# Optimization experiments

Measured on AMD Instinct MI355X. Metric: run time of the kernel, lower is better.

The kernel has to match this reference:

```python
import jax, jax.numpy as jnp
import numpy as np

N, E, D, H = 50000, 400000, 128, 256


def setup_inputs() -> dict:
    key = jax.random.key(0)
    ks = jax.random.split(key, 16)
    s = 0.02
    inp = {
        "x": jax.random.normal(ks[0], (N, D), dtype=jnp.float32),
        "edge_index": jax.random.randint(ks[1], (2, E), 0, N, dtype=jnp.int64),
        "steps": 1,
        # encoder MLP: Linear(D->H), Linear(H->H), relu after each
        "enc_w1": jax.random.normal(ks[2], (H, D), dtype=jnp.float32) * s,
        "enc_b1": jnp.zeros((H,), dtype=jnp.float32),
        "enc_w2": jax.random.normal(ks[3], (H, H), dtype=jnp.float32) * s,
        "enc_b2": jnp.zeros((H,), dtype=jnp.float32),
        # GeneralConv lin_msg (root_weight=False, bias=True)
        "msg_w": jax.random.normal(ks[4], (H, H), dtype=jnp.float32) * s,
        "msg_b": jnp.zeros((H,), dtype=jnp.float32),
        # decoder MLP: Linear(2H->H) relu, Linear(H->D) tanh
        "dec_w1": jax.random.normal(ks[5], (H, 2 * H), dtype=jnp.float32) * s,
        "dec_b1": jnp.zeros((H,), dtype=jnp.float32),
        "dec_w2": jax.random.normal(ks[6], (D, H), dtype=jnp.float32) * s,
        "dec_b2": jnp.zeros((D,), dtype=jnp.float32),
    }
    return inp


def reference(x, edge_index, steps, enc_w1, enc_b1, enc_w2, enc_b2,
              msg_w, msg_b, dec_w1, dec_b1, dec_w2, dec_b2):
    src = edge_index[0]
    dst = edge_index[1]
    n = x.shape[0]
    for _ in range(steps):  # steps is a small static python int
        # encoder MLP (batch_norm=False, dropout=0, relu + relu)
        h = jax.nn.relu(x @ enc_w1.T + enc_b1)
        h = jax.nn.relu(h @ enc_w2.T + enc_b2)
        # GeneralConv: message = lin_msg(x_j); aggr='add'; no root weight
        # lin_msg is edge-independent -> transform on nodes, then gather/scatter
        m = h @ msg_w.T + msg_b                      # [N, H]
        out = jax.ops.segment_sum(m[src], dst, num_segments=n)  # [N, H]
        # decoder on cat(out, h): relu then tanh
        d = jax.nn.relu(jnp.concatenate([out, h], axis=-1) @ dec_w1.T + dec_b1)
        x = jnp.tanh(d @ dec_w2.T + dec_b2)
    return x
```

## Files before the change

### kernel.cpp

```cpp
#include <hip/hip_runtime.h>
#include <cmath>


typedef __attribute__((ext_vector_type(8))) short  short8;
typedef __attribute__((ext_vector_type(4))) float  f32x4;
typedef __attribute__((ext_vector_type(4))) unsigned short us4;

typedef unsigned short u16;
typedef unsigned int   u32;

static __device__ __forceinline__ u16 f2bf(float f) {
    u32 u = __float_as_uint(f);
    u = (u + 0x7FFFu + ((u >> 16) & 1u)) >> 16;
    return (u16)u;
}
static __device__ __forceinline__ float bf2f(u16 h) {
    return __uint_as_float(((u32)h) << 16);
}

static __device__ __forceinline__ void g2l16(const void* g, void* l) {
    __builtin_amdgcn_global_load_lds(
        (const __attribute__((address_space(1))) u32*)g,
        (__attribute__((address_space(3))) u32*)l, 16, 0, 0);
}

__global__ __launch_bounds__(256, 2) void enc_fused(
    const u16* __restrict__ xb, const u16* __restrict__ w1,
    const float* __restrict__ b1, const u16* __restrict__ w2,
    const float* __restrict__ b2, const u16* __restrict__ wm,
    const float* __restrict__ bm, u16* __restrict__ hout,
    u16* __restrict__ mout, const int N)
{
    __shared__ u16 As[64 * 32];
    __shared__ u16 Ws[256 * 32];
    __shared__ u16 hL[8][64 * 32];

    const int t    = threadIdx.x;
    const int r0   = blockIdx.x * 64;
    const int wave = t >> 6;
    const int lane = t & 63;
    const int n    = lane & 15;
    const int q    = lane >> 4;
    const int wc   = wave * 64;
    const int lrow = lane >> 2;
    const int qofs = (lane & 3) * 8;

    const int arow = min(r0 + wave * 16 + lrow, N - 1);
    const u16* aptr = xb + (size_t)arow * 128 + qofs;

    int wrow[4];
#pragma unroll
    for (int k2 = 0; k2 < 4; k2++) wrow[k2] = (wave + 4 * k2) * 16 + lrow;

    f32x4 acc[4][4];
#pragma unroll
    for (int i = 0; i < 4; i++)
#pragma unroll
        for (int j = 0; j < 4; j++) acc[i][j] = (f32x4)0.0f;

    for (int kc = 0; kc < 128; kc += 32) {
        __syncthreads();
        g2l16(aptr + kc, &As[wave * 512]);
#pragma unroll
        for (int k2 = 0; k2 < 4; k2++)
            g2l16(w1 + (size_t)wrow[k2] * 128 + kc + qofs,
                  &Ws[(wave + 4 * k2) * 512]);
        __syncthreads();
        short8 af[4], bf[4];
#pragma unroll
        for (int i = 0; i < 4; i++)
            af[i] = *reinterpret_cast<const short8*>(&As[(i * 16 + n) * 32 + q * 8]);
#pragma unroll
        for (int j = 0; j < 4; j++)
            bf[j] = *reinterpret_cast<const short8*>(&Ws[(wc + j * 16 + n) * 32 + q * 8]);
#pragma unroll
        for (int i = 0; i < 4; i++)
#pragma unroll
            for (int j = 0; j < 4; j++)
                acc[i][j] = __builtin_amdgcn_mfma_f32_16x16x32_bf16(
                    af[i], bf[j], acc[i][j], 0, 0, 0);
    }
    {
        float bv[4];
#pragma unroll
        for (int j = 0; j < 4; j++) bv[j] = b1[wc + j * 16 + n];
#pragma unroll
        for (int i = 0; i < 4; i++)
#pragma unroll
            for (int reg = 0; reg < 4; reg++) {
                const int row = i * 16 + q * 4 + reg;
#pragma unroll
                for (int j = 0; j < 4; j++) {
                    const int col = wc + j * 16 + n;
                    const float v = fmaxf(acc[i][j][reg] + bv[j], 0.0f);
                    hL[col >> 5][row * 32 + (col & 31)] = f2bf(v);
                }
            }
    }

#pragma unroll
    for (int i = 0; i < 4; i++)
#pragma unroll
        for (int j = 0; j < 4; j++) acc[i][j] = (f32x4)0.0f;
    for (int c = 0; c < 8; c++) {
        __syncthreads();
#pragma unroll
        for (int k2 = 0; k2 < 4; k2++)
            g2l16(w2 + (size_t)wrow[k2] * 256 + c * 32 + qofs,
                  &Ws[(wave + 4 * k2) * 512]);
        __syncthreads();
        short8 af[4], bf[4];
#pragma unroll
        for (int i = 0; i < 4; i++)
            af[i] = *reinterpret_cast<const short8*>(&hL[c][(i * 16 + n) * 32 + q * 8]);
#pragma unroll
        for (int j = 0; j < 4; j++)
            bf[j] = *reinterpret_cast<const short8*>(&Ws[(wc + j * 16 + n) * 32 + q * 8]);
#pragma unroll
        for (int i = 0; i < 4; i++)
#pragma unroll
            for (int j = 0; j < 4; j++)
                acc[i][j] = __builtin_amdgcn_mfma_f32_16x16x32_bf16(
                    af[i], bf[j], acc[i][j], 0, 0, 0);
    }
    {
        float bv[4];
#pragma unroll
        for (int j = 0; j < 4; j++) bv[j] = b2[wc + j * 16 + n];
#pragma unroll
        for (int i = 0; i < 4; i++)
#pragma unroll
            for (int reg = 0; reg < 4; reg++) {
                const int row = r0 + i * 16 + q * 4 + reg;
                if (row < N) {
#pragma unroll
                    for (int j = 0; j < 4; j++) {
                        const float v = fmaxf(acc[i][j][reg] + bv[j], 0.0f);
                        hout[(size_t)row * 256 + wc + j * 16 + n] = f2bf(v);
                    }
                }
            }
        __syncthreads();
#pragma unroll
        for (int i = 0; i < 4; i++)
#pragma unroll
            for (int reg = 0; reg < 4; reg++) {
                const int row = i * 16 + q * 4 + reg;
#pragma unroll
                for (int j = 0; j < 4; j++) {
                    const int col = wc + j * 16 + n;
                    const float v = fmaxf(acc[i][j][reg] + bv[j], 0.0f);
                    hL[col >> 5][row * 32 + (col & 31)] = f2bf(v);
                }
            }
    }

#pragma unroll
    for (int i = 0; i < 4; i++)
#pragma unroll
        for (int j = 0; j < 4; j++) acc[i][j] = (f32x4)0.0f;
    for (int c = 0; c < 8; c++) {
        __syncthreads();
#pragma unroll
        for (int k2 = 0; k2 < 4; k2++)
            g2l16(wm + (size_t)wrow[k2] * 256 + c * 32 + qofs,
                  &Ws[(wave + 4 * k2) * 512]);
        __syncthreads();
        short8 af[4], bf[4];
#pragma unroll
        for (int i = 0; i < 4; i++)
            af[i] = *reinterpret_cast<const short8*>(&hL[c][(i * 16 + n) * 32 + q * 8]);
#pragma unroll
        for (int j = 0; j < 4; j++)
            bf[j] = *reinterpret_cast<const short8*>(&Ws[(wc + j * 16 + n) * 32 + q * 8]);
#pragma unroll
        for (int i = 0; i < 4; i++)
#pragma unroll
            for (int j = 0; j < 4; j++)
                acc[i][j] = __builtin_amdgcn_mfma_f32_16x16x32_bf16(
                    af[i], bf[j], acc[i][j], 0, 0, 0);
    }
    {
        float bv[4];
#pragma unroll
        for (int j = 0; j < 4; j++) bv[j] = bm[wc + j * 16 + n];
#pragma unroll
        for (int i = 0; i < 4; i++)
#pragma unroll
            for (int reg = 0; reg < 4; reg++) {
                const int row = r0 + i * 16 + q * 4 + reg;
                if (row < N) {
#pragma unroll
                    for (int j = 0; j < 4; j++)
                        mout[(size_t)row * 256 + wc + j * 16 + n] =
                            f2bf(acc[i][j][reg] + bv[j]);
                }
            }
    }
}

__global__ __launch_bounds__(256, 2) void dec_fused(
    const u16* __restrict__ aggr, const u16* __restrict__ h,
    const u16* __restrict__ wd1, const float* __restrict__ bd1,
    const u16* __restrict__ wd2, const float* __restrict__ bd2,
    float* __restrict__ out, const int N)
{
    __shared__ u16 As[64 * 32];
    __shared__ u16 Ws[256 * 32];
    __shared__ u16 dL[8][64 * 32];

    const int t    = threadIdx.x;
    const int r0   = blockIdx.x * 64;
    const int wave = t >> 6;
    const int lane = t & 63;
    const int n    = lane & 15;
    const int q    = lane >> 4;
    const int wc   = wave * 64;
    const int lrow = lane >> 2;
    const int qofs = (lane & 3) * 8;

    const int arow = min(r0 + wave * 16 + lrow, N - 1);
    const u16* ap0 = aggr + (size_t)arow * 256 + qofs;
    const u16* ap1 = h    + (size_t)arow * 256 + qofs;

    int wrow[4];
#pragma unroll
    for (int k2 = 0; k2 < 4; k2++) wrow[k2] = (wave + 4 * k2) * 16 + lrow;

    f32x4 acc[4][4];
#pragma unroll
    for (int i = 0; i < 4; i++)
#pragma unroll
        for (int j = 0; j < 4; j++) acc[i][j] = (f32x4)0.0f;

    for (int kc = 0; kc < 512; kc += 32) {
        __syncthreads();
        if (kc < 256) g2l16(ap0 + kc, &As[wave * 512]);
        else          g2l16(ap1 + (kc - 256), &As[wave * 512]);
#pragma unroll
        for (int k2 = 0; k2 < 4; k2++)
            g2l16(wd1 + (size_t)wrow[k2] * 512 + kc + qofs,
                  &Ws[(wave + 4 * k2) * 512]);
        __syncthreads();
        short8 af[4], bf[4];
#pragma unroll
        for (int i = 0; i < 4; i++)
            af[i] = *reinterpret_cast<const short8*>(&As[(i * 16 + n) * 32 + q * 8]);
#pragma unroll
        for (int j = 0; j < 4; j++)
            bf[j] = *reinterpret_cast<const short8*>(&Ws[(wc + j * 16 + n) * 32 + q * 8]);
#pragma unroll
        for (int i = 0; i < 4; i++)
#pragma unroll
            for (int j = 0; j < 4; j++)
                acc[i][j] = __builtin_amdgcn_mfma_f32_16x16x32_bf16(
                    af[i], bf[j], acc[i][j], 0, 0, 0);
    }
    {
        float bv[4];
#pragma unroll
        for (int j = 0; j < 4; j++) bv[j] = bd1[wc + j * 16 + n];
#pragma unroll
        for (int i = 0; i < 4; i++)
#pragma unroll
            for (int reg = 0; reg < 4; reg++) {
                const int row = i * 16 + q * 4 + reg;
#pragma unroll
                for (int j = 0; j < 4; j++) {
                    const int col = wc + j * 16 + n;
                    const float v = fmaxf(acc[i][j][reg] + bv[j], 0.0f);
                    dL[col >> 5][row * 32 + (col & 31)] = f2bf(v);
                }
            }
    }

    f32x4 acc2[4][2];
#pragma unroll
    for (int i = 0; i < 4; i++)
#pragma unroll
        for (int j = 0; j < 2; j++) acc2[i][j] = (f32x4)0.0f;
    const int wc2 = wave * 32;
    for (int c = 0; c < 8; c++) {
        __syncthreads();
        g2l16(wd2 + (size_t)(wave * 16 + lrow) * 256 + c * 32 + qofs,
              &Ws[wave * 512]);
        g2l16(wd2 + (size_t)((wave + 4) * 16 + lrow) * 256 + c * 32 + qofs,
              &Ws[(wave + 4) * 512]);
        __syncthreads();
        short8 af[4], bf[2];
#pragma unroll
        for (int i = 0; i < 4; i++)
            af[i] = *reinterpret_cast<const short8*>(&dL[c][(i * 16 + n) * 32 + q * 8]);
#pragma unroll
        for (int j = 0; j < 2; j++)
            bf[j] = *reinterpret_cast<const short8*>(&Ws[(wc2 + j * 16 + n) * 32 + q * 8]);
#pragma unroll
        for (int i = 0; i < 4; i++)
#pragma unroll
            for (int j = 0; j < 2; j++)
                acc2[i][j] = __builtin_amdgcn_mfma_f32_16x16x32_bf16(
                    af[i], bf[j], acc2[i][j], 0, 0, 0);
    }
    {
        float bv[2];
#pragma unroll
        for (int j = 0; j < 2; j++) bv[j] = bd2[wc2 + j * 16 + n];
#pragma unroll
        for (int i = 0; i < 4; i++)
#pragma unroll
            for (int reg = 0; reg < 4; reg++) {
                const int row = r0 + i * 16 + q * 4 + reg;
                if (row < N) {
#pragma unroll
                    for (int j = 0; j < 2; j++)
                        out[(size_t)row * 128 + wc2 + j * 16 + n] =
                            tanhf(acc2[i][j][reg] + bv[j]);
                }
            }
    }
}

__global__ __launch_bounds__(256) void cvt7_kernel(
    const float* s0, const float* s1, const float* s2, const float* s3,
    const float* s4, const float* s5,
    u16* d0, u16* d1, u16* d2, u16* d3, u16* d4, u16* d5,
    int* __restrict__ zp,
    int n0, int n1, int n2, int n3, int n4, int n5, int nz)
{
    const int i = blockIdx.x * 256 + threadIdx.x;
    if (blockIdx.y == 6) {
        if (i < nz) zp[i] = 0;
        return;
    }
    const float* s; u16* d; int nq;
    switch (blockIdx.y) {
        case 0: s = s0; d = d0; nq = n0; break;
        case 1: s = s1; d = d1; nq = n1; break;
        case 2: s = s2; d = d2; nq = n2; break;
        case 3: s = s3; d = d3; nq = n3; break;
        case 4: s = s4; d = d4; nq = n4; break;
        default: s = s5; d = d5; nq = n5; break;
    }
    if (i < nq) {
        const float4 v = reinterpret_cast<const float4*>(s)[i];
        us4 o = { f2bf(v.x), f2bf(v.y), f2bf(v.z), f2bf(v.w) };
        reinterpret_cast<us4*>(d)[i] = o;
    }
}

__global__ __launch_bounds__(256) void fill_kernel(
    const int* __restrict__ ei, int* __restrict__ cursor,
    int* __restrict__ bucket, const int E, const int Nn)
{
    const int e = blockIdx.x * 256 + threadIdx.x;
    if (e < E) {
        const int src = ei[e];
        const int dst = ei[(size_t)E + e];
        if ((unsigned)dst < (unsigned)Nn) {
            const int pos = atomicAdd(&cursor[dst], 1);
            if (pos < 64) bucket[(size_t)dst * 64 + pos] = src;
        }
    }
}

__global__ __launch_bounds__(256) void gather_sum_kernel(
    const u16* __restrict__ m, const int* __restrict__ bucket,
    const int* __restrict__ cursor, u16* __restrict__ outa, const int Nn)
{
    const int wave = (int)((blockIdx.x * 256u + threadIdx.x) >> 6);
    const int lane = threadIdx.x & 63;
    if (wave >= Nn) return;
    const int cnt = min(cursor[wave], 64);
    const int* bl = bucket + (size_t)wave * 64;
    float a0 = 0.f, a1 = 0.f, a2 = 0.f, a3 = 0.f;
    int i = 0;
    for (; i + 3 < cnt; i += 4) {
        int sidx[4];
#pragma unroll
        for (int u = 0; u < 4; u++) sidx[u] = bl[i + u];
        us4 v[4];
#pragma unroll
        for (int u = 0; u < 4; u++) {
            const int s = ((unsigned)sidx[u] < (unsigned)Nn) ? sidx[u] : 0;
            v[u] = *reinterpret_cast<const us4*>(&m[(size_t)s * 256 + lane * 4]);
        }
#pragma unroll
        for (int u = 0; u < 4; u++) {
            if ((unsigned)sidx[u] < (unsigned)Nn) {
                a0 += bf2f(v[u].x); a1 += bf2f(v[u].y);
                a2 += bf2f(v[u].z); a3 += bf2f(v[u].w);
            }
        }
    }
    for (; i < cnt; i++) {
        const int s0 = bl[i];
        if ((unsigned)s0 < (unsigned)Nn) {
            const us4 v0 = *reinterpret_cast<const us4*>(
                &m[(size_t)s0 * 256 + lane * 4]);
            a0 += bf2f(v0.x); a1 += bf2f(v0.y);
            a2 += bf2f(v0.z); a3 += bf2f(v0.w);
        }
    }
    us4 o = { f2bf(a0), f2bf(a1), f2bf(a2), f2bf(a3) };
    *reinterpret_cast<us4*>(&outa[(size_t)wave * 256 + lane * 4]) = o;
}

extern "C" void kernel_launch(void* const* d_in, const int* in_sizes, int n_in,
                              void* d_out, int out_size, void* d_ws, size_t ws_size,
                              hipStream_t stream)
{
    const float* x      = (const float*)d_in[0];
    const int*   ei     = (const int*)d_in[1];
    const float* enc_w1 = (const float*)d_in[3];
    const float* enc_b1 = (const float*)d_in[4];
    const float* enc_w2 = (const float*)d_in[5];
    const float* enc_b2 = (const float*)d_in[6];
    const float* msg_w  = (const float*)d_in[7];
    const float* msg_b  = (const float*)d_in[8];
    const float* dec_w1 = (const float*)d_in[9];
    const float* dec_b1 = (const float*)d_in[10];
    const float* dec_w2 = (const float*)d_in[11];
    const float* dec_b2 = (const float*)d_in[12];

    const int N = 50000, D = 128, H = 256;
    const int E = in_sizes[1] / 2;

    u16* xb   = (u16*)d_ws;
    u16* h    = xb   + (size_t)N * D;
    u16* m    = h    + (size_t)N * H;
    u16* aggr = m    + (size_t)N * H;
    u16* w1   = aggr + (size_t)N * H;
    u16* w2   = w1 + 256 * 128;
    u16* wm   = w2 + 256 * 256;
    u16* wd1  = wm + 256 * 256;
    u16* wd2  = wd1 + 256 * 512;
    int* cursor = (int*)(wd2 + 128 * 256);
    int* bucket = cursor + N;

    const dim3 blk(256);
    const int nb64 = (N + 63) / 64;

    cvt7_kernel<<<dim3((N * D / 4 + 255) / 256, 7), blk, 0, stream>>>(
        x, enc_w1, enc_w2, msg_w, dec_w1, dec_w2,
        xb, w1, w2, wm, wd1, wd2, cursor,
        N * D / 4, 256 * 128 / 4, 256 * 256 / 4, 256 * 256 / 4,
        256 * 512 / 4, 128 * 256 / 4, N);

    fill_kernel<<<dim3((E + 255) / 256), blk, 0, stream>>>(
        ei, cursor, bucket, E, N);

    enc_fused<<<dim3(nb64), blk, 0, stream>>>(
        xb, w1, enc_b1, w2, enc_b2, wm, msg_b, h, m, N);

    gather_sum_kernel<<<dim3((N * 64 + 255) / 256), blk, 0, stream>>>(
        m, bucket, cursor, aggr, N);

    dec_fused<<<dim3(nb64), blk, 0, stream>>>(
        aggr, h, wd1, dec_b1, wd2, dec_b2, (float*)d_out, N);
}
```

Before: 246.0 us.

## Fuse neighbor gather-sum into decoder kernel via LDS-staged aggregate tile

Removes the standalone gather_sum kernel. Each decoder block now gathers and sums the neighbor messages for its 64 nodes straight into shared memory, then consumes them as the first half of the dec_w1 GEMM K dimension. This drops the aggr buffer's global write and read and one kernel launch. In exchange, the gather latency now runs inside a GEMM block with launch_bounds(256,2), so there are fewer waves in flight to hide the random gather loads.

After: 294.3 us. +19.6%, slower.

```diff
diff --git a/kernel.cpp b/kernel.cpp
--- a/kernel.cpp
+++ b/kernel.cpp
@@ -199,15 +199,16 @@
     }
 }
 
-__global__ __launch_bounds__(256, 2) void dec_fused(
-    const u16* __restrict__ aggr, const u16* __restrict__ h,
+__global__ __launch_bounds__(256, 2) void dec_gather(
+    const u16* __restrict__ m, const int* __restrict__ bucket,
+    const int* __restrict__ cursor, const u16* __restrict__ h,
     const u16* __restrict__ wd1, const float* __restrict__ bd1,
     const u16* __restrict__ wd2, const float* __restrict__ bd2,
     float* __restrict__ out, const int N)
 {
+    __shared__ u16 AL[8][64 * 32];
+    __shared__ u16 Ws[256 * 32];
     __shared__ u16 As[64 * 32];
-    __shared__ u16 Ws[256 * 32];
-    __shared__ u16 dL[8][64 * 32];
 
     const int t    = threadIdx.x;
     const int r0   = blockIdx.x * 64;
@@ -219,10 +220,53 @@
     const int lrow = lane >> 2;
     const int qofs = (lane & 3) * 8;
 
+    {
+        const int cchunk = lane >> 3;
+        const int ccol   = (lane & 7) * 4;
+        for (int k = 0; k < 16; k++) {
+            const int lr   = wave * 16 + k;
+            const int node = r0 + lr;
+            float a0 = 0.f, a1 = 0.f, a2 = 0.f, a3 = 0.f;
+            if (node < N) {
+                const int cnt = min(cursor[node], 64);
+                const int* bl = bucket + (size_t)node * 64;
+                int i = 0;
+                for (; i + 3 < cnt; i += 4) {
+                    int sidx[4];
+#pragma unroll
+                    for (int u = 0; u < 4; u++) sidx[u] = bl[i + u];
+                    us4 v[4];
+#pragma unroll
+                    for (int u = 0; u < 4; u++) {
+                        const int s = ((unsigned)sidx[u] < (unsigned)N) ? sidx[u] : 0;
+                        v[u] = *reinterpret_cast<const us4*>(
+                            &m[(size_t)s * 256 + lane * 4]);
+                    }
+#pragma unroll
+                    for (int u = 0; u < 4; u++) {
+                        if ((unsigned)sidx[u] < (unsigned)N) {
+                            a0 += bf2f(v[u].x); a1 += bf2f(v[u].y);
+                            a2 += bf2f(v[u].z); a3 += bf2f(v[u].w);
+                        }
+                    }
+                }
+                for (; i < cnt; i++) {
+                    const int s0 = bl[i];
+                    if ((unsigned)s0 < (unsigned)N) {
+                        const us4 v0 = *reinterpret_cast<const us4*>(
+                            &m[(size_t)s0 * 256 + lane * 4]);
+                        a0 += bf2f(v0.x); a1 += bf2f(v0.y);
+                        a2 += bf2f(v0.z); a3 += bf2f(v0.w);
+                    }
+                }
+            }
+            us4 o = { f2bf(a0), f2bf(a1), f2bf(a2), f2bf(a3) };
+            *reinterpret_cast<us4*>(&AL[cchunk][lr * 32 + ccol]) = o;
+        }
+    }
+
     const int arow = min(r0 + wave * 16 + lrow, N - 1);
-    const u16* ap0 = aggr + (size_t)arow * 256 + qofs;
-    const u16* ap1 = h    + (size_t)arow * 256 + qofs;
-
+    const u16* hp = h + (size_t)arow * 256 + qofs;
     int wrow[4];
 #pragma unroll
     for (int k2 = 0; k2 < 4; k2++) wrow[k2] = (wave + 4 * k2) * 16 + lrow;
@@ -233,19 +277,17 @@
 #pragma unroll
         for (int j = 0; j < 4; j++) acc[i][j] = (f32x4)0.0f;
 
-    for (int kc = 0; kc < 512; kc += 32) {
-        __syncthreads();
-        if (kc < 256) g2l16(ap0 + kc, &As[wave * 512]);
-        else          g2l16(ap1 + (kc - 256), &As[wave * 512]);
+    for (int c = 0; c < 8; c++) {
+        __syncthreads();
 #pragma unroll
         for (int k2 = 0; k2 < 4; k2++)
-            g2l16(wd1 + (size_t)wrow[k2] * 512 + kc + qofs,
+            g2l16(wd1 + (size_t)wrow[k2] * 512 + c * 32 + qofs,
                   &Ws[(wave + 4 * k2) * 512]);
         __syncthreads();
         short8 af[4], bf[4];
 #pragma unroll
         for (int i = 0; i < 4; i++)
-            af[i] = *reinterpret_cast<const short8*>(&As[(i * 16 + n) * 32 + q * 8]);
+            af[i] = *reinterpret_cast<const short8*>(&AL[c][(i * 16 + n) * 32 + q * 8]);
 #pragma unroll
         for (int j = 0; j < 4; j++)
             bf[j] = *reinterpret_cast<const short8*>(&Ws[(wc + j * 16 + n) * 32 + q * 8]);
@@ -256,6 +298,28 @@
                 acc[i][j] = __builtin_amdgcn_mfma_f32_16x16x32_bf16(
                     af[i], bf[j], acc[i][j], 0, 0, 0);
     }
+    for (int c = 8; c < 16; c++) {
+        __syncthreads();
+        g2l16(hp + (c - 8) * 32, &As[wave * 512]);
+#pragma unroll
+        for (int k2 = 0; k2 < 4; k2++)
+            g2l16(wd1 + (size_t)wrow[k2] * 512 + c * 32 + qofs,
+                  &Ws[(wave + 4 * k2) * 512]);
+        __syncthreads();
+        short8 af[4], bf[4];
+#pragma unroll
+        for (int i = 0; i < 4; i++)
+            af[i] = *reinterpret_cast<const short8*>(&As[(i * 16 + n) * 32 + q * 8]);
+#pragma unroll
+        for (int j = 0; j < 4; j++)
+            bf[j] = *reinterpret_cast<const short8*>(&Ws[(wc + j * 16 + n) * 32 + q * 8]);
+#pragma unroll
+        for (int i = 0; i < 4; i++)
+#pragma unroll
+            for (int j = 0; j < 4; j++)
+                acc[i][j] = __builtin_amdgcn_mfma_f32_16x16x32_bf16(
+                    af[i], bf[j], acc[i][j], 0, 0, 0);
+    }
     {
         float bv[4];
 #pragma unroll
@@ -269,7 +333,7 @@
                 for (int j = 0; j < 4; j++) {
                     const int col = wc + j * 16 + n;
                     const float v = fmaxf(acc[i][j][reg] + bv[j], 0.0f);
-                    dL[col >> 5][row * 32 + (col & 31)] = f2bf(v);
+                    AL[col >> 5][row * 32 + (col & 31)] = f2bf(v);
                 }
             }
     }
@@ -290,7 +354,7 @@
         short8 af[4], bf[2];
 #pragma unroll
         for (int i = 0; i < 4; i++)
-            af[i] = *reinterpret_cast<const short8*>(&dL[c][(i * 16 + n) * 32 + q * 8]);
+            af[i] = *reinterpret_cast<const short8*>(&AL[c][(i * 16 + n) * 32 + q * 8]);
 #pragma unroll
         for (int j = 0; j < 2; j++)
             bf[j] = *reinterpret_cast<const short8*>(&Ws[(wc2 + j * 16 + n) * 32 + q * 8]);
@@ -361,48 +425,6 @@
             if (pos < 64) bucket[(size_t)dst * 64 + pos] = src;
         }
     }
-}
-
-__global__ __launch_bounds__(256) void gather_sum_kernel(
-    const u16* __restrict__ m, const int* __restrict__ bucket,
-    const int* __restrict__ cursor, u16* __restrict__ outa, const int Nn)
-{
-    const int wave = (int)((blockIdx.x * 256u + threadIdx.x) >> 6);
-    const int lane = threadIdx.x & 63;
-    if (wave >= Nn) return;
-    const int cnt = min(cursor[wave], 64);
-    const int* bl = bucket + (size_t)wave * 64;
-    float a0 = 0.f, a1 = 0.f, a2 = 0.f, a3 = 0.f;
-    int i = 0;
-    for (; i + 3 < cnt; i += 4) {
-        int sidx[4];
-#pragma unroll
-        for (int u = 0; u < 4; u++) sidx[u] = bl[i + u];
-        us4 v[4];
-#pragma unroll
-        for (int u = 0; u < 4; u++) {
-            const int s = ((unsigned)sidx[u] < (unsigned)Nn) ? sidx[u] : 0;
-            v[u] = *reinterpret_cast<const us4*>(&m[(size_t)s * 256 + lane * 4]);
-        }
-#pragma unroll
-        for (int u = 0; u < 4; u++) {
-            if ((unsigned)sidx[u] < (unsigned)Nn) {
-                a0 += bf2f(v[u].x); a1 += bf2f(v[u].y);
-                a2 += bf2f(v[u].z); a3 += bf2f(v[u].w);
-            }
-        }
-    }
-    for (; i < cnt; i++) {
-        const int s0 = bl[i];
-        if ((unsigned)s0 < (unsigned)Nn) {
-            const us4 v0 = *reinterpret_cast<const us4*>(
-                &m[(size_t)s0 * 256 + lane * 4]);
-            a0 += bf2f(v0.x); a1 += bf2f(v0.y);
-            a2 += bf2f(v0.z); a3 += bf2f(v0.w);
-        }
-    }
-    us4 o = { f2bf(a0), f2bf(a1), f2bf(a2), f2bf(a3) };
-    *reinterpret_cast<us4*>(&outa[(size_t)wave * 256 + lane * 4]) = o;
 }
 
 extern "C" void kernel_launch(void* const* d_in, const int* in_sizes, int n_in,
@@ -428,8 +450,7 @@
     u16* xb   = (u16*)d_ws;
     u16* h    = xb   + (size_t)N * D;
     u16* m    = h    + (size_t)N * H;
-    u16* aggr = m    + (size_t)N * H;
-    u16* w1   = aggr + (size_t)N * H;
+    u16* w1   = m    + (size_t)N * H;
     u16* w2   = w1 + 256 * 128;
     u16* wm   = w2 + 256 * 256;
     u16* wd1  = wm + 256 * 256;
@@ -452,9 +473,6 @@
     enc_fused<<<dim3(nb64), blk, 0, stream>>>(
         xb, w1, enc_b1, w2, enc_b2, wm, msg_b, h, m, N);
 
-    gather_sum_kernel<<<dim3((N * 64 + 255) / 256), blk, 0, stream>>>(
-        m, bucket, cursor, aggr, N);
-
-    dec_fused<<<dim3(nb64), blk, 0, stream>>>(
-        aggr, h, wd1, dec_b1, wd2, dec_b2, (float*)d_out, N);
-}
+    dec_gather<<<dim3(nb64), blk, 0, stream>>>(
+        m, bucket, cursor, h, wd1, dec_b1, wd2, dec_b2, (float*)d_out, N);
+}
```

## Use 8 waves per block in encoder and decoder GEMM kernels

Applied to the files above, without the earlier changes.

Doubles the block size of the fused encoder and decoder kernels from 256 to 512 threads. Each wave now computes a 32-column slice instead of 64, which halves the per-wave accumulator registers and spreads the weight-tile loads over more waves. The aim is more latency hiding and lower register pressure for the same 64-row tile. The trade-off is heavier per-barrier synchronisation, and some waves sit idle during the A-tile loads.

Measured after the change: 244.8 us. Within noise of the previous version (-0.5%).

```diff
diff --git a/kernel.cpp b/kernel.cpp
--- a/kernel.cpp
+++ b/kernel.cpp
@@ -24,7 +24,7 @@
         (__attribute__((address_space(3))) u32*)l, 16, 0, 0);
 }
 
-__global__ __launch_bounds__(256, 2) void enc_fused(
+__global__ __launch_bounds__(512, 2) void enc_fused(
     const u16* __restrict__ xb, const u16* __restrict__ w1,
     const float* __restrict__ b1, const u16* __restrict__ w2,
     const float* __restrict__ b2, const u16* __restrict__ wm,
@@ -41,59 +41,54 @@
     const int lane = t & 63;
     const int n    = lane & 15;
     const int q    = lane >> 4;
-    const int wc   = wave * 64;
+    const int wc   = wave * 32;
     const int lrow = lane >> 2;
     const int qofs = (lane & 3) * 8;
 
     const int arow = min(r0 + wave * 16 + lrow, N - 1);
     const u16* aptr = xb + (size_t)arow * 128 + qofs;
-
-    int wrow[4];
-#pragma unroll
-    for (int k2 = 0; k2 < 4; k2++) wrow[k2] = (wave + 4 * k2) * 16 + lrow;
-
-    f32x4 acc[4][4];
+    const int wrA = wave * 16 + lrow;
+    const int wrB = (wave + 8) * 16 + lrow;
+
+    f32x4 acc[4][2];
 #pragma unroll
     for (int i = 0; i < 4; i++)
 #pragma unroll
-        for (int j = 0; j < 4; j++) acc[i][j] = (f32x4)0.0f;
+        for (int j = 0; j < 2; j++) acc[i][j] = (f32x4)0.0f;
 
     for (int kc = 0; kc < 128; kc += 32) {
         __syncthreads();
-        g2l16(aptr + kc, &As[wave * 512]);
-#pragma unroll
-        for (int k2 = 0; k2 < 4; k2++)
-            g2l16(w1 + (size_t)wrow[k2] * 128 + kc + qofs,
-                  &Ws[(wave + 4 * k2) * 512]);
-        __syncthreads();
-        short8 af[4], bf[4];
+        if (wave < 4) g2l16(aptr + kc, &As[wave * 512]);
+        g2l16(w1 + (size_t)wrA * 128 + kc + qofs, &Ws[wave * 512]);
+        g2l16(w1 + (size_t)wrB * 128 + kc + qofs, &Ws[(wave + 8) * 512]);
+        __syncthreads();
+        short8 af[4], bf[2];
 #pragma unroll
         for (int i = 0; i < 4; i++)
             af[i] = *reinterpret_cast<const short8*>(&As[(i * 16 + n) * 32 + q * 8]);
 #pragma unroll
-        for (int j = 0; j < 4; j++)
+        for (int j = 0; j < 2; j++)
             bf[j] = *reinterpret_cast<const short8*>(&Ws[(wc + j * 16 + n) * 32 + q * 8]);
 #pragma unroll
         for (int i = 0; i < 4; i++)
 #pragma unroll
-            for (int j = 0; j < 4; j++)
+            for (int j = 0; j < 2; j++)
                 acc[i][j] = __builtin_amdgcn_mfma_f32_16x16x32_bf16(
                     af[i], bf[j], acc[i][j], 0, 0, 0);
     }
     {
-        float bv[4];
-#pragma unroll
-        for (int j = 0; j < 4; j++) bv[j] = b1[wc + j * 16 + n];
+        float bv[2];
+#pragma unroll
+        for (int j = 0; j < 2; j++) bv[j] = b1[wc + j * 16 + n];
 #pragma unroll
         for (int i = 0; i < 4; i++)
 #pragma unroll
             for (int reg = 0; reg < 4; reg++) {
                 const int row = i * 16 + q * 4 + reg;
 #pragma unroll
-                for (int j = 0; j < 4; j++) {
-                    const int col = wc + j * 16 + n;
+                for (int j = 0; j < 2; j++) {
                     const float v = fmaxf(acc[i][j][reg] + bv[j], 0.0f);
-                    hL[col >> 5][row * 32 + (col & 31)] = f2bf(v);
+                    hL[wave][row * 32 + j * 16 + n] = f2bf(v);
                 }
             }
     }
@@ -101,32 +96,30 @@
 #pragma unroll
     for (int i = 0; i < 4; i++)
 #pragma unroll
-        for (int j = 0; j < 4; j++) acc[i][j] = (f32x4)0.0f;
+        for (int j = 0; j < 2; j++) acc[i][j] = (f32x4)0.0f;
     for (int c = 0; c < 8; c++) {
         __syncthreads();
-#pragma unroll
-        for (int k2 = 0; k2 < 4; k2++)
-            g2l16(w2 + (size_t)wrow[k2] * 256 + c * 32 + qofs,
-                  &Ws[(wave + 4 * k2) * 512]);
-        __syncthreads();
-        short8 af[4], bf[4];
+        g2l16(w2 + (size_t)wrA * 256 + c * 32 + qofs, &Ws[wave * 512]);
+        g2l16(w2 + (size_t)wrB * 256 + c * 32 + qofs, &Ws[(wave + 8) * 512]);
+        __syncthreads();
+        short8 af[4], bf[2];
 #pragma unroll
         for (int i = 0; i < 4; i++)
             af[i] = *reinterpret_cast<const short8*>(&hL[c][(i * 16 + n) * 32 + q * 8]);
 #pragma unroll
-        for (int j = 0; j < 4; j++)
+        for (int j = 0; j < 2; j++)
             bf[j] = *reinterpret_cast<const short8*>(&Ws[(wc + j * 16 + n) * 32 + q * 8]);
 #pragma unroll
         for (int i = 0; i < 4; i++)
 #pragma unroll
-            for (int j = 0; j < 4; j++)
+            for (int j = 0; j < 2; j++)
                 acc[i][j] = __builtin_amdgcn_mfma_f32_16x16x32_bf16(
                     af[i], bf[j], acc[i][j], 0, 0, 0);
     }
     {
-        float bv[4];
-#pragma unroll
-        for (int j = 0; j < 4; j++) bv[j] = b2[wc + j * 16 + n];
+        float bv[2];
+#pragma unroll
+        for (int j = 0; j < 2; j++) bv[j] = b2[wc + j * 16 + n];
 #pragma unroll
         for (int i = 0; i < 4; i++)
 #pragma unroll
@@ -134,7 +127,7 @@
                 const int row = r0 + i * 16 + q * 4 + reg;
                 if (row < N) {
 #pragma unroll
-                    for (int j = 0; j < 4; j++) {
+                    for (int j = 0; j < 2; j++) {
                         const float v = fmaxf(acc[i][j][reg] + bv[j], 0.0f);
                         hout[(size_t)row * 256 + wc + j * 16 + n] = f2bf(v);
                     }
@@ -147,10 +140,9 @@
             for (int reg = 0; reg < 4; reg++) {
                 const int row = i * 16 + q * 4 + reg;
 #pragma unroll
-                for (int j = 0; j < 4; j++) {
-                    const int col = wc + j * 16 + n;
+                for (int j = 0; j < 2; j++) {
                     const float v = fmaxf(acc[i][j][reg] + bv[j], 0.0f);
-                    hL[col >> 5][row * 32 + (col & 31)] = f2bf(v);
+                    hL[wave][row * 32 + j * 16 + n] = f2bf(v);
                 }
             }
     }
@@ -158,32 +150,30 @@
 #pragma unroll
     for (int i = 0; i < 4; i++)
 #pragma unroll
-        for (int j = 0; j < 4; j++) acc[i][j] = (f32x4)0.0f;
+        for (int j = 0; j < 2; j++) acc[i][j] = (f32x4)0.0f;
     for (int c = 0; c < 8; c++) {
         __syncthreads();
-#pragma unroll
-        for (int k2 = 0; k2 < 4; k2++)
-            g2l16(wm + (size_t)wrow[k2] * 256 + c * 32 + qofs,
-                  &Ws[(wave + 4 * k2) * 512]);
-        __syncthreads();
-        short8 af[4], bf[4];
+        g2l16(wm + (size_t)wrA * 256 + c * 32 + qofs, &Ws[wave * 512]);
+        g2l16(wm + (size_t)wrB * 256 + c * 32 + qofs, &Ws[(wave + 8) * 512]);
+        __syncthreads();
+        short8 af[4], bf[2];
 #pragma unroll
         for (int i = 0; i < 4; i++)
             af[i] = *reinterpret_cast<const short8*>(&hL[c][(i * 16 + n) * 32 + q * 8]);
 #pragma unroll
-        for (int j = 0; j < 4; j++)
+        for (int j = 0; j < 2; j++)
             bf[j] = *reinterpret_cast<const short8*>(&Ws[(wc + j * 16 + n) * 32 + q * 8]);
 #pragma unroll
         for (int i = 0; i < 4; i++)
 #pragma unroll
-            for (int j = 0; j < 4; j++)
+            for (int j = 0; j < 2; j++)
                 acc[i][j] = __builtin_amdgcn_mfma_f32_16x16x32_bf16(
                     af[i], bf[j], acc[i][j], 0, 0, 0);
     }
     {
-        float bv[4];
-#pragma unroll
-        for (int j = 0; j < 4; j++) bv[j] = bm[wc + j * 16 + n];
+        float bv[2];
+#pragma unroll
+        for (int j = 0; j < 2; j++) bv[j] = bm[wc + j * 16 + n];
 #pragma unroll
         for (int i = 0; i < 4; i++)
 #pragma unroll
@@ -191,7 +181,7 @@
                 const int row = r0 + i * 16 + q * 4 + reg;
                 if (row < N) {
 #pragma unroll
-                    for (int j = 0; j < 4; j++)
+                    for (int j = 0; j < 2; j++)
                         mout[(size_t)row * 256 + wc + j * 16 + n] =
                             f2bf(acc[i][j][reg] + bv[j]);
                 }
@@ -199,7 +189,7 @@
     }
 }
 
-__global__ __launch_bounds__(256, 2) void dec_fused(
+__global__ __launch_bounds__(512, 2) void dec_fused(
     const u16* __restrict__ aggr, const u16* __restrict__ h,
     const u16* __restrict__ wd1, const float* __restrict__ bd1,
     const u16* __restrict__ wd2, const float* __restrict__ bd2,
@@ -215,107 +205,90 @@
     const int lane = t & 63;
     const int n    = lane & 15;
     const int q    = lane >> 4;
-    const int wc   = wave * 64;
+    const int wc   = wave * 32;
     const int lrow = lane >> 2;
     const int qofs = (lane & 3) * 8;
 
     const int arow = min(r0 + wave * 16 + lrow, N - 1);
     const u16* ap0 = aggr + (size_t)arow * 256 + qofs;
     const u16* ap1 = h    + (size_t)arow * 256 + qofs;
-
-    int wrow[4];
-#pragma unroll
-    for (int k2 = 0; k2 < 4; k2++) wrow[k2] = (wave + 4 * k2) * 16 + lrow;
-
-    f32x4 acc[4][4];
+    const int wrA = wave * 16 + lrow;
+    const int wrB = (wave + 8) * 16 + lrow;
+
+    f32x4 acc[4][2];
 #pragma unroll
     for (int i = 0; i < 4; i++)
 #pragma unroll
-        for (int j = 0; j < 4; j++) acc[i][j] = (f32x4)0.0f;
+        for (int j = 0; j < 2; j++) acc[i][j] = (f32x4)0.0f;
 
     for (int kc = 0; kc < 512; kc += 32) {
         __syncthreads();
-        if (kc < 256) g2l16(ap0 + kc, &As[wave * 512]);
-        else          g2l16(ap1 + (kc - 256), &As[wave * 512]);
-#pragma unroll
-        for (int k2 = 0; k2 < 4; k2++)
-            g2l16(wd1 + (size_t)wrow[k2] * 512 + kc + qofs,
-                  &Ws[(wave + 4 * k2) * 512]);
-        __syncthreads();
-        short8 af[4], bf[4];
+        if (wave < 4) {
+            if (kc < 256) g2l16(ap0 + kc, &As[wave * 512]);
+            else          g2l16(ap1 + (kc - 256), &As[wave * 512]);
+        }
+        g2l16(wd1 + (size_t)wrA * 512 + kc + qofs, &Ws[wave * 512]);
+        g2l16(wd1 + (size_t)wrB * 512 + kc + qofs, &Ws[(wave + 8) * 512]);
+        __syncthreads();
+        short8 af[4], bf[2];
 #pragma unroll
         for (int i = 0; i < 4; i++)
             af[i] = *reinterpret_cast<const short8*>(&As[(i * 16 + n) * 32 + q * 8]);
 #pragma unroll
-        for (int j = 0; j < 4; j++)
+        for (int j = 0; j < 2; j++)
             bf[j] = *reinterpret_cast<const short8*>(&Ws[(wc + j * 16 + n) * 32 + q * 8]);
 #pragma unroll
         for (int i = 0; i < 4; i++)
 #pragma unroll
-            for (int j = 0; j < 4; j++)
+            for (int j = 0; j < 2; j++)
                 acc[i][j] = __builtin_amdgcn_mfma_f32_16x16x32_bf16(
                     af[i], bf[j], acc[i][j], 0, 0, 0);
     }
     {
-        float bv[4];
-#pragma unroll
-        for (int j = 0; j < 4; j++) bv[j] = bd1[wc + j * 16 + n];
+        float bv[2];
+#pragma unroll
+        for (int j = 0; j < 2; j++) bv[j] = bd1[wc + j * 16 + n];
 #pragma unroll
         for (int i = 0; i < 4; i++)
 #pragma unroll
             for (int reg = 0; reg < 4; reg++) {
                 const int row = i * 16 + q * 4 + reg;
 #pragma unroll
-                for (int j = 0; j < 4; j++) {
-                    const int col = wc + j * 16 + n;
+                for (int j = 0; j < 2; j++) {
                     const float v = fmaxf(acc[i][j][reg] + bv[j], 0.0f);
-                    dL[col >> 5][row * 32 + (col & 31)] = f2bf(v);
+                    dL[wave][row * 32 + j * 16 + n] = f2bf(v);
                 }
             }
     }
 
-    f32x4 acc2[4][2];
-#pragma unroll
-    for (int i = 0; i < 4; i++)
-#pragma unroll
-        for (int j = 0; j < 2; j++) acc2[i][j] = (f32x4)0.0f;
-    const int wc2 = wave * 32;
+    f32x4 acc2[4];
+#pragma unroll
+    for (int i = 0; i < 4; i++) acc2[i] = (f32x4)0.0f;
+    const int wc2 = wave * 16;
     for (int c = 0; c < 8; c++) {
         __syncthreads();
         g2l16(wd2 + (size_t)(wave * 16 + lrow) * 256 + c * 32 + qofs,
               &Ws[wave * 512]);
-        g2l16(wd2 + (size_t)((wave + 4) * 16 + lrow) * 256 + c * 32 + qofs,
-              &Ws[(wave + 4) * 512]);
-        __syncthreads();
-        short8 af[4], bf[2];
+        __syncthreads();
+        short8 af[4], bf;
 #pragma unroll
         for (int i = 0; i < 4; i++)
             af[i] = *reinterpret_cast<const short8*>(&dL[c][(i * 16 + n) * 32 + q * 8]);
-#pragma unroll
-        for (int j = 0; j < 2; j++)
-            bf[j] = *reinterpret_cast<const short8*>(&Ws[(wc2 + j * 16 + n) * 32 + q * 8]);
-#pragma unroll
-        for (int i = 0; i < 4; i++)
-#pragma unroll
-            for (int j = 0; j < 2; j++)
-                acc2[i][j] = __builtin_amdgcn_mfma_f32_16x16x32_bf16(
-                    af[i], bf[j], acc2[i][j], 0, 0, 0);
+        bf = *reinterpret_cast<const short8*>(&Ws[(wave * 16 + n) * 32 + q * 8]);
+#pragma unroll
+        for (int i = 0; i < 4; i++)
+            acc2[i] = __builtin_amdgcn_mfma_f32_16x16x32_bf16(
+                af[i], bf, acc2[i], 0, 0, 0);
     }
     {
-        float bv[2];
-#pragma unroll
-        for (int j = 0; j < 2; j++) bv[j] = bd2[wc2 + j * 16 + n];
+        const float bv = bd2[wc2 + n];
 #pragma unroll
         for (int i = 0; i < 4; i++)
 #pragma unroll
             for (int reg = 0; reg < 4; reg++) {
                 const int row = r0 + i * 16 + q * 4 + reg;
-                if (row < N) {
-#pragma unroll
-                    for (int j = 0; j < 2; j++)
-                        out[(size_t)row * 128 + wc2 + j * 16 + n] =
-                            tanhf(acc2[i][j][reg] + bv[j]);
-                }
+                if (row < N)
+                    out[(size_t)row * 128 + wc2 + n] = tanhf(acc2[i][reg] + bv);
             }
     }
 }
@@ -438,6 +411,7 @@
     int* bucket = cursor + N;
 
     const dim3 blk(256);
+    const dim3 blk512(512);
     const int nb64 = (N + 63) / 64;
 
     cvt7_kernel<<<dim3((N * D / 4 + 255) / 256, 7), blk, 0, stream>>>(
@@ -449,12 +423,12 @@
     fill_kernel<<<dim3((E + 255) / 256), blk, 0, stream>>>(
         ei, cursor, bucket, E, N);
 
-    enc_fused<<<dim3(nb64), blk, 0, stream>>>(
+    enc_fused<<<dim3(nb64), blk512, 0, stream>>>(
         xb, w1, enc_b1, w2, enc_b2, wm, msg_b, h, m, N);
 
     gather_sum_kernel<<<dim3((N * 64 + 255) / 256), blk, 0, stream>>>(
         m, bucket, cursor, aggr, N);
 
-    dec_fused<<<dim3(nb64), blk, 0, stream>>>(
+    dec_fused<<<dim3(nb64), blk512, 0, stream>>>(
         aggr, h, wd1, dec_b1, wd2, dec_b2, (float*)d_out, N);
 }
```

## Load MFMA operands directly from global memory instead of staging through LDS

Applied to the files above, without the earlier changes.

The encoder and decoder GEMM loops no longer stage the input rows and weight tiles through shared memory with global_load_lds and per-chunk barriers. Each wave now loads its MFMA fragments straight from global memory, relying on L1/L2 to serve the weights shared across waves, and the K loops are fully unrolled with one barrier per layer. The launch-bounds occupancy hint of 2 is dropped. This removes the many __syncthreads and LDS round trips, but it issues redundant global loads and leaves no explicit prefetching.

Result: slower. 286.7 us (+16.5%).

```diff
diff --git a/kernel.cpp b/kernel.cpp
--- a/kernel.cpp
+++ b/kernel.cpp
@@ -17,22 +17,17 @@
 static __device__ __forceinline__ float bf2f(u16 h) {
     return __uint_as_float(((u32)h) << 16);
 }
-
-static __device__ __forceinline__ void g2l16(const void* g, void* l) {
-    __builtin_amdgcn_global_load_lds(
-        (const __attribute__((address_space(1))) u32*)g,
-        (__attribute__((address_space(3))) u32*)l, 16, 0, 0);
-}
-
-__global__ __launch_bounds__(256, 2) void enc_fused(
+static __device__ __forceinline__ short8 ld8(const u16* p) {
+    return *reinterpret_cast<const short8*>(p);
+}
+
+__global__ __launch_bounds__(256) void enc_fused(
     const u16* __restrict__ xb, const u16* __restrict__ w1,
     const float* __restrict__ b1, const u16* __restrict__ w2,
     const float* __restrict__ b2, const u16* __restrict__ wm,
     const float* __restrict__ bm, u16* __restrict__ hout,
     u16* __restrict__ mout, const int N)
 {
-    __shared__ u16 As[64 * 32];
-    __shared__ u16 Ws[256 * 32];
     __shared__ u16 hL[8][64 * 32];
 
     const int t    = threadIdx.x;
@@ -42,15 +37,14 @@
     const int n    = lane & 15;
     const int q    = lane >> 4;
     const int wc   = wave * 64;
-    const int lrow = lane >> 2;
-    const int qofs = (lane & 3) * 8;
-
-    const int arow = min(r0 + wave * 16 + lrow, N - 1);
-    const u16* aptr = xb + (size_t)arow * 128 + qofs;
-
-    int wrow[4];
-#pragma unroll
-    for (int k2 = 0; k2 < 4; k2++) wrow[k2] = (wave + 4 * k2) * 16 + lrow;
+
+    const u16* ax[4];
+#pragma unroll
+    for (int i = 0; i < 4; i++)
+        ax[i] = xb + (size_t)min(r0 + i * 16 + n, N - 1) * 128 + q * 8;
+    int brow[4];
+#pragma unroll
+    for (int j = 0; j < 4; j++) brow[j] = wc + j * 16 + n;
 
     f32x4 acc[4][4];
 #pragma unroll
@@ -58,21 +52,14 @@
 #pragma unroll
         for (int j = 0; j < 4; j++) acc[i][j] = (f32x4)0.0f;
 
-    for (int kc = 0; kc < 128; kc += 32) {
-        __syncthreads();
-        g2l16(aptr + kc, &As[wave * 512]);
-#pragma unroll
-        for (int k2 = 0; k2 < 4; k2++)
-            g2l16(w1 + (size_t)wrow[k2] * 128 + kc + qofs,
-                  &Ws[(wave + 4 * k2) * 512]);
-        __syncthreads();
+#pragma unroll
+    for (int c = 0; c < 4; c++) {
         short8 af[4], bf[4];
 #pragma unroll
-        for (int i = 0; i < 4; i++)
-            af[i] = *reinterpret_cast<const short8*>(&As[(i * 16 + n) * 32 + q * 8]);
+        for (int i = 0; i < 4; i++) af[i] = ld8(ax[i] + c * 32);
 #pragma unroll
         for (int j = 0; j < 4; j++)
-            bf[j] = *reinterpret_cast<const short8*>(&Ws[(wc + j * 16 + n) * 32 + q * 8]);
+            bf[j] = ld8(w1 + (size_t)brow[j] * 128 + c * 32 + q * 8);
 #pragma unroll
         for (int i = 0; i < 4; i++)
 #pragma unroll
@@ -97,25 +84,21 @@
                 }
             }
     }
+    __syncthreads();
 
 #pragma unroll
     for (int i = 0; i < 4; i++)
 #pragma unroll
         for (int j = 0; j < 4; j++) acc[i][j] = (f32x4)0.0f;
+#pragma unroll
     for (int c = 0; c < 8; c++) {
-        __syncthreads();
-#pragma unroll
-        for (int k2 = 0; k2 < 4; k2++)
-            g2l16(w2 + (size_t)wrow[k2] * 256 + c * 32 + qofs,
-                  &Ws[(wave + 4 * k2) * 512]);
-        __syncthreads();
         short8 af[4], bf[4];
 #pragma unroll
         for (int i = 0; i < 4; i++)
-            af[i] = *reinterpret_cast<const short8*>(&hL[c][(i * 16 + n) * 32 + q * 8]);
+            af[i] = ld8(&hL[c][(i * 16 + n) * 32 + q * 8]);
 #pragma unroll
         for (int j = 0; j < 4; j++)
-            bf[j] = *reinterpret_cast<const short8*>(&Ws[(wc + j * 16 + n) * 32 + q * 8]);
+            bf[j] = ld8(w2 + (size_t)brow[j] * 256 + c * 32 + q * 8);
 #pragma unroll
         for (int i = 0; i < 4; i++)
 #pragma unroll
@@ -154,25 +137,21 @@
                 }
             }
     }
+    __syncthreads();
 
 #pragma unroll
     for (int i = 0; i < 4; i++)
 #pragma unroll
         for (int j = 0; j < 4; j++) acc[i][j] = (f32x4)0.0f;
+#pragma unroll
     for (int c = 0; c < 8; c++) {
-        __syncthreads();
-#pragma unroll
-        for (int k2 = 0; k2 < 4; k2++)
-            g2l16(wm + (size_t)wrow[k2] * 256 + c * 32 + qofs,
-                  &Ws[(wave + 4 * k2) * 512]);
-        __syncthreads();
         short8 af[4], bf[4];
 #pragma unroll
         for (int i = 0; i < 4; i++)
-            af[i] = *reinterpret_cast<const short8*>(&hL[c][(i * 16 + n) * 32 + q * 8]);
+            af[i] = ld8(&hL[c][(i * 16 + n) * 32 + q * 8]);
 #pragma unroll
         for (int j = 0; j < 4; j++)
-            bf[j] = *reinterpret_cast<const short8*>(&Ws[(wc + j * 16 + n) * 32 + q * 8]);
+            bf[j] = ld8(wm + (size_t)brow[j] * 256 + c * 32 + q * 8);
 #pragma unroll
         for (int i = 0; i < 4; i++)
 #pragma unroll
@@ -199,14 +178,12 @@
     }
 }
 
-__global__ __launch_bounds__(256, 2) void dec_fused(
+__global__ __launch_bounds__(256) void dec_fused(
     const u16* __restrict__ aggr, const u16* __restrict__ h,
     const u16* __restrict__ wd1, const float* __restrict__ bd1,
     const u16* __restrict__ wd2, const float* __restrict__ bd2,
     float* __restrict__ out, const int N)
 {
-    __shared__ u16 As[64 * 32];
-    __shared__ u16 Ws[256 * 32];
     __shared__ u16 dL[8][64 * 32];
 
     const int t    = threadIdx.x;
@@ -216,16 +193,18 @@
     const int n    = lane & 15;
     const int q    = lane >> 4;
     const int wc   = wave * 64;
-    const int lrow = lane >> 2;
-    const int qofs = (lane & 3) * 8;
-
-    const int arow = min(r0 + wave * 16 + lrow, N - 1);
-    const u16* ap0 = aggr + (size_t)arow * 256 + qofs;
-    const u16* ap1 = h    + (size_t)arow * 256 + qofs;
-
-    int wrow[4];
-#pragma unroll
-    for (int k2 = 0; k2 < 4; k2++) wrow[k2] = (wave + 4 * k2) * 16 + lrow;
+
+    const u16* aa[4];
+    const u16* ah[4];
+#pragma unroll
+    for (int i = 0; i < 4; i++) {
+        const size_t row = (size_t)min(r0 + i * 16 + n, N - 1);
+        aa[i] = aggr + row * 256 + q * 8;
+        ah[i] = h    + row * 256 + q * 8;
+    }
+    int brow[4];
+#pragma unroll
+    for (int j = 0; j < 4; j++) brow[j] = wc + j * 16 + n;
 
     f32x4 acc[4][4];
 #pragma unroll
@@ -233,22 +212,15 @@
 #pragma unroll
         for (int j = 0; j < 4; j++) acc[i][j] = (f32x4)0.0f;
 
-    for (int kc = 0; kc < 512; kc += 32) {
-        __syncthreads();
-        if (kc < 256) g2l16(ap0 + kc, &As[wave * 512]);
-        else          g2l16(ap1 + (kc - 256), &As[wave * 512]);
-#pragma unroll
-        for (int k2 = 0; k2 < 4; k2++)
-            g2l16(wd1 + (size_t)wrow[k2] * 512 + kc + qofs,
-                  &Ws[(wave + 4 * k2) * 512]);
-        __syncthreads();
+#pragma unroll
+    for (int c = 0; c < 16; c++) {
         short8 af[4], bf[4];
 #pragma unroll
         for (int i = 0; i < 4; i++)
-            af[i] = *reinterpret_cast<const short8*>(&As[(i * 16 + n) * 32 + q * 8]);
+            af[i] = (c < 8) ? ld8(aa[i] + c * 32) : ld8(ah[i] + (c - 8) * 32);
 #pragma unroll
         for (int j = 0; j < 4; j++)
-            bf[j] = *reinterpret_cast<const short8*>(&Ws[(wc + j * 16 + n) * 32 + q * 8]);
+            bf[j] = ld8(wd1 + (size_t)brow[j] * 512 + c * 32 + q * 8);
 #pragma unroll
         for (int i = 0; i < 4; i++)
 #pragma unroll
@@ -273,6 +245,7 @@
                 }
             }
     }
+    __syncthreads();
 
     f32x4 acc2[4][2];
 #pragma unroll
@@ -280,20 +253,15 @@
 #pragma unroll
         for (int j = 0; j < 2; j++) acc2[i][j] = (f32x4)0.0f;
     const int wc2 = wave * 32;
+#pragma unroll
     for (int c = 0; c < 8; c++) {
-        __syncthreads();
-        g2l16(wd2 + (size_t)(wave * 16 + lrow) * 256 + c * 32 + qofs,
-              &Ws[wave * 512]);
-        g2l16(wd2 + (size_t)((wave + 4) * 16 + lrow) * 256 + c * 32 + qofs,
-              &Ws[(wave + 4) * 512]);
-        __syncthreads();
         short8 af[4], bf[2];
 #pragma unroll
         for (int i = 0; i < 4; i++)
-            af[i] = *reinterpret_cast<const short8*>(&dL[c][(i * 16 + n) * 32 + q * 8]);
+            af[i] = ld8(&dL[c][(i * 16 + n) * 32 + q * 8]);
 #pragma unroll
         for (int j = 0; j < 2; j++)
-            bf[j] = *reinterpret_cast<const short8*>(&Ws[(wc2 + j * 16 + n) * 32 + q * 8]);
+            bf[j] = ld8(wd2 + (size_t)(wc2 + j * 16 + n) * 256 + c * 32 + q * 8);
 #pragma unroll
         for (int i = 0; i < 4; i++)
 #pragma unroll
```
